# Kernel optimization log

Hardware: AMD Instinct MI355X
Metric: run time of the kernel (lower is better)

The kernel has to match this reference:

```python
import jax, jax.numpy as jnp
import numpy as np

N_NODES = 50000
N_EDGES = 800000
D = 64  # node_in = edge_out = node_out

def _mlp(h, w1, b1, w2, b2):
    h = jax.nn.relu(h @ w1 + b1)
    return h @ w2 + b2

def setup_inputs() -> dict:
    key = jax.random.key(0)
    ks = jax.random.split(key, 12)
    def lin(k, fan_in, fan_out):
        bound = 1.0 / np.sqrt(fan_in)
        kw, kb = jax.random.split(k)
        w = jax.random.uniform(kw, (fan_in, fan_out), jnp.float32, -bound, bound)
        b = jax.random.uniform(kb, (fan_out,), jnp.float32, -bound, bound)
        return w, b
    x = jax.random.normal(ks[0], (N_NODES, D), jnp.float32)
    edge_index = jax.random.randint(ks[1], (2, N_EDGES), 0, N_NODES, jnp.int64 if jax.config.jax_enable_x64 else jnp.int32)
    edge_attr = jax.random.normal(ks[2], (N_EDGES, D), jnp.float32)
    u = jax.random.normal(ks[3], (1, D), jnp.float32)
    batch = jnp.zeros((N_NODES,), dtype=edge_index.dtype)
    w1a, b1a = lin(ks[4], 2 * D, D)
    w1b, b1b = lin(ks[5], D, D)
    w2a, b2a = lin(ks[6], 2 * D, D)
    w2b, b2b = lin(ks[7], D, D)
    return dict(x=x, edge_index=edge_index, edge_attr=edge_attr, u=u, batch=batch,
                w1a=w1a, b1a=b1a, w1b=w1b, b1b=b1b,
                w2a=w2a, b2a=b2a, w2b=w2b, b2b=b2b)

def reference(x, edge_index, edge_attr, u, batch,
              w1a, b1a, w1b, b1b, w2a, b2a, w2b, b2b):
    row, col = edge_index[0], edge_index[1]
    n = x.shape[0]
    # gather source nodes, concat with edge features: [E, node_in+edge_out]
    h = jnp.concatenate([x[row], edge_attr], axis=1)
    h = _mlp(h, w1a, b1a, w1b, b1b)
    # scatter_mean over destination nodes (zeros for nodes with no incoming edges)
    summed = jax.ops.segment_sum(h, col, num_segments=n)  # [N, D]
    counts = jax.ops.segment_sum(jnp.ones((h.shape[0],), h.dtype), col, num_segments=n)
    agg = summed / jnp.maximum(counts, 1.0)[:, None]
    out = jnp.concatenate([x, agg], axis=1)
    return _mlp(out, w2a, b2a, w2b, b2b)
```

## Files before the change

kernel.cpp:

```cpp
#include <hip/hip_runtime.h>

#define DF 64

typedef __attribute__((ext_vector_type(8))) short bf16x8;
typedef __attribute__((ext_vector_type(2))) short v2s;
typedef __attribute__((ext_vector_type(4))) float f32x4;

__device__ __forceinline__ short f2bf(float f) {
    union { float f; unsigned u; } v; v.f = f;
    unsigned u = v.u;
    u += 0x7FFFu + ((u >> 16) & 1u);
    return (short)(u >> 16);
}

__device__ __forceinline__ float bf2f(unsigned s) {
    union { unsigned u; float f; } v; v.u = s << 16;
    return v.f;
}

__device__ __forceinline__ bf16x8 cvt8(float4 a, float4 b) {
    bf16x8 r;
    r[0] = f2bf(a.x); r[1] = f2bf(a.y); r[2] = f2bf(a.z); r[3] = f2bf(a.w);
    r[4] = f2bf(b.x); r[5] = f2bf(b.y); r[6] = f2bf(b.z); r[7] = f2bf(b.w);
    return r;
}

__device__ __forceinline__ void wave_lds_sync() {
    asm volatile("s_waitcnt lgkmcnt(0)" ::: "memory");
    __builtin_amdgcn_sched_barrier(0);
}

__device__ __forceinline__ void pk_add(short* addr, int val) {
#if __has_builtin(__builtin_amdgcn_global_atomic_fadd_v2bf16)
    __builtin_amdgcn_global_atomic_fadd_v2bf16(
        (__attribute__((address_space(1))) v2s*)addr, *(v2s*)&val);
#else
    unsigned* a = (unsigned*)addr;
    unsigned old = *a, assumed;
    do {
        assumed = old;
        float lo = bf2f(assumed & 0xffffu) + bf2f((unsigned)val & 0xffffu);
        float hi = bf2f(assumed >> 16)     + bf2f((unsigned)val >> 16);
        unsigned nv = (unsigned)(unsigned short)f2bf(lo) |
                      ((unsigned)(unsigned short)f2bf(hi) << 16);
        old = atomicCAS(a, assumed, nv);
    } while (old != assumed);
#endif
}

__global__ __launch_bounds__(256) void prep_weights(
    const float* __restrict__ w1a, const float* __restrict__ w1b,
    const float* __restrict__ w2a, const float* __restrict__ w2b,
    short* __restrict__ w1aT, short* __restrict__ w1bT,
    short* __restrict__ w2aT, short* __restrict__ w2bT)
{
    int gid = blockIdx.x * 256 + threadIdx.x;
    if (gid < 8192) {
        int k = gid >> 6, n = gid & 63;
        w1aT[n * 128 + k] = f2bf(w1a[gid]);
    } else if (gid < 12288) {
        int g = gid - 8192; int k = g >> 6, n = g & 63;
        w1bT[n * 64 + k] = f2bf(w1b[g]);
    } else if (gid < 20480) {
        int g = gid - 12288; int k = g >> 6, n = g & 63;
        w2aT[n * 128 + k] = f2bf(w2a[g]);
    } else if (gid < 24576) {
        int g = gid - 20480; int k = g >> 6, n = g & 63;
        w2bT[n * 64 + k] = f2bf(w2b[g]);
    }
}

__global__ __launch_bounds__(256, 4) void edge_mlp_scatter(
    const float* __restrict__ x, const int* __restrict__ ei,
    const float* __restrict__ ea,
    const short* __restrict__ w1aT, const float* __restrict__ b1a,
    const short* __restrict__ w1bT, const float* __restrict__ b1b,
    short* __restrict__ summedh, float* __restrict__ counts, int E)
{
    __shared__ alignas(16) short lsH[4 * 2 * 16 * 72];

    const int t = threadIdx.x;
    const int lane = t & 63;
    const int w = t >> 6;
    const int q = lane >> 4;
    const int m = lane & 15;
    const long base = ((long)blockIdx.x * 4 + w) * 32;

    const long e0 = base + m;
    const long e1 = base + 16 + m;
    const long ec0 = e0 < E ? e0 : (long)(E - 1);
    const long ec1 = e1 < E ? e1 : (long)(E - 1);
    const int row0 = ei[ec0];
    const int row1 = ei[ec1];

    if (q == 0) {
        if (e0 < E) unsafeAtomicAdd(&counts[ei[E + e0]], 1.0f);
        if (e1 < E) unsafeAtomicAdd(&counts[ei[E + e1]], 1.0f);
    }

    const float4* xr0 = (const float4*)(x + (long)row0 * DF);
    const float4* er0 = (const float4*)(ea + ec0 * DF);
    const float4* xr1 = (const float4*)(x + (long)row1 * DF);
    const float4* er1 = (const float4*)(ea + ec1 * DF);

    float4 ax0 = xr0[q * 2],     ax1 = xr0[q * 2 + 1];
    float4 ax2 = xr0[8 + q * 2], ax3 = xr0[8 + q * 2 + 1];
    float4 ae0 = er0[q * 2],     ae1 = er0[q * 2 + 1];
    float4 ae2 = er0[8 + q * 2], ae3 = er0[8 + q * 2 + 1];
    float4 bx0 = xr1[q * 2],     bx1 = xr1[q * 2 + 1];
    float4 bx2 = xr1[8 + q * 2], bx3 = xr1[8 + q * 2 + 1];
    float4 be0 = er1[q * 2],     be1 = er1[q * 2 + 1];
    float4 be2 = er1[8 + q * 2], be3 = er1[8 + q * 2 + 1];

    bf16x8 afr0[4], afr1[4];
    afr0[0] = cvt8(ax0, ax1); afr0[1] = cvt8(ax2, ax3);
    afr0[2] = cvt8(ae0, ae1); afr0[3] = cvt8(ae2, ae3);
    afr1[0] = cvt8(bx0, bx1); afr1[1] = cvt8(bx2, bx3);
    afr1[2] = cvt8(be0, be1); afr1[3] = cvt8(be2, be3);

    f32x4 acc0[4], acc1[4];
#pragma unroll
    for (int nt = 0; nt < 4; ++nt) {
        float b = b1a[nt * 16 + m];
        f32x4 v = {b, b, b, b};
        acc0[nt] = v; acc1[nt] = v;
#pragma unroll
        for (int ks = 0; ks < 4; ++ks) {
            bf16x8 wf = *(const bf16x8*)&w1aT[(nt * 16 + m) * 128 + ks * 32 + q * 8];
            acc0[nt] = __builtin_amdgcn_mfma_f32_16x16x32_bf16(afr0[ks], wf, acc0[nt], 0, 0, 0);
            acc1[nt] = __builtin_amdgcn_mfma_f32_16x16x32_bf16(afr1[ks], wf, acc1[nt], 0, 0, 0);
        }
    }

    short* hw0 = lsH + w * (2 * 16 * 72);
    short* hw1 = hw0 + 16 * 72;
#pragma unroll
    for (int nt = 0; nt < 4; ++nt)
#pragma unroll
        for (int r = 0; r < 4; ++r) {
            float v0 = acc0[nt][r] > 0.f ? acc0[nt][r] : 0.f;
            float v1 = acc1[nt][r] > 0.f ? acc1[nt][r] : 0.f;
            hw0[(q * 4 + r) * 72 + nt * 16 + m] = f2bf(v0);
            hw1[(q * 4 + r) * 72 + nt * 16 + m] = f2bf(v1);
        }
    wave_lds_sync();

    bf16x8 a20[2], a21[2];
    a20[0] = *(const bf16x8*)&hw0[m * 72 + q * 8];
    a20[1] = *(const bf16x8*)&hw0[m * 72 + 32 + q * 8];
    a21[0] = *(const bf16x8*)&hw1[m * 72 + q * 8];
    a21[1] = *(const bf16x8*)&hw1[m * 72 + 32 + q * 8];

    f32x4 acd0[4], acd1[4];
#pragma unroll
    for (int nt = 0; nt < 4; ++nt) {
        float b = b1b[nt * 16 + m];
        f32x4 v = {b, b, b, b};
        acd0[nt] = v; acd1[nt] = v;
#pragma unroll
        for (int ks = 0; ks < 2; ++ks) {
            bf16x8 wf = *(const bf16x8*)&w1bT[(nt * 16 + m) * 64 + ks * 32 + q * 8];
            acd0[nt] = __builtin_amdgcn_mfma_f32_16x16x32_bf16(a20[ks], wf, acd0[nt], 0, 0, 0);
            acd1[nt] = __builtin_amdgcn_mfma_f32_16x16x32_bf16(a21[ks], wf, acd1[nt], 0, 0, 0);
        }
    }
    wave_lds_sync();

#pragma unroll
    for (int nt = 0; nt < 4; ++nt)
#pragma unroll
        for (int r = 0; r < 4; ++r) {
            hw0[(q * 4 + r) * 72 + nt * 16 + m] = f2bf(acd0[nt][r]);
            hw1[(q * 4 + r) * 72 + nt * 16 + m] = f2bf(acd1[nt][r]);
        }
    wave_lds_sync();

    const int p = lane & 31;
    const int* hwi0 = (const int*)hw0;
    const int* hwi1 = (const int*)hw1;
#pragma unroll
    for (int i = 0; i < 8; ++i) {
        int r2 = (lane >> 5) + 2 * i;
        long eg0 = base + r2;
        long eg1 = base + 16 + r2;
        if (eg0 < E) {
            int dst = ei[E + eg0];
            pk_add(&summedh[(long)dst * DF + 2 * p], hwi0[r2 * 36 + p]);
        }
        if (eg1 < E) {
            int dst = ei[E + eg1];
            pk_add(&summedh[(long)dst * DF + 2 * p], hwi1[r2 * 36 + p]);
        }
    }
}

__global__ __launch_bounds__(256, 4) void node_mlp(
    const float* __restrict__ x, const short* __restrict__ summedh,
    const float* __restrict__ counts,
    const short* __restrict__ w2aT, const float* __restrict__ b2a,
    const short* __restrict__ w2bT, const float* __restrict__ b2b,
    float* __restrict__ out, int NN)
{
    __shared__ alignas(16) short lsH[4 * 2 * 16 * 72];

    const int t = threadIdx.x;
    const int lane = t & 63;
    const int w = t >> 6;
    const int q = lane >> 4;
    const int m = lane & 15;
    const long base = ((long)blockIdx.x * 4 + w) * 32;

    const long n0 = base + m;
    const long n1 = base + 16 + m;
    const long nc0 = n0 < NN ? n0 : (long)(NN - 1);
    const long nc1 = n1 < NN ? n1 : (long)(NN - 1);

    const float4* xr0 = (const float4*)(x + nc0 * DF);
    const float4* xr1 = (const float4*)(x + nc1 * DF);

    float4 ax0 = xr0[q * 2],     ax1 = xr0[q * 2 + 1];
    float4 ax2 = xr0[8 + q * 2], ax3 = xr0[8 + q * 2 + 1];
    float4 bx0 = xr1[q * 2],     bx1 = xr1[q * 2 + 1];
    float4 bx2 = xr1[8 + q * 2], bx3 = xr1[8 + q * 2 + 1];
    bf16x8 s00 = *(const bf16x8*)&summedh[nc0 * DF + q * 8];
    bf16x8 s01 = *(const bf16x8*)&summedh[nc0 * DF + 32 + q * 8];
    bf16x8 s10 = *(const bf16x8*)&summedh[nc1 * DF + q * 8];
    bf16x8 s11 = *(const bf16x8*)&summedh[nc1 * DF + 32 + q * 8];
    float c0 = counts[nc0];
    float c1 = counts[nc1];
    c0 = c0 > 1.f ? c0 : 1.f;
    c1 = c1 > 1.f ? c1 : 1.f;
    const float inv0 = 1.f / c0;
    const float inv1 = 1.f / c1;

    bf16x8 afr0[4], afr1[4];
    afr0[0] = cvt8(ax0, ax1); afr0[1] = cvt8(ax2, ax3);
    afr1[0] = cvt8(bx0, bx1); afr1[1] = cvt8(bx2, bx3);
#pragma unroll
    for (int i = 0; i < 8; ++i) {
        afr0[2][i] = f2bf(bf2f((unsigned short)s00[i]) * inv0);
        afr0[3][i] = f2bf(bf2f((unsigned short)s01[i]) * inv0);
        afr1[2][i] = f2bf(bf2f((unsigned short)s10[i]) * inv1);
        afr1[3][i] = f2bf(bf2f((unsigned short)s11[i]) * inv1);
    }

    f32x4 acc0[4], acc1[4];
#pragma unroll
    for (int nt = 0; nt < 4; ++nt) {
        float b = b2a[nt * 16 + m];
        f32x4 v = {b, b, b, b};
        acc0[nt] = v; acc1[nt] = v;
#pragma unroll
        for (int ks = 0; ks < 4; ++ks) {
            bf16x8 wf = *(const bf16x8*)&w2aT[(nt * 16 + m) * 128 + ks * 32 + q * 8];
            acc0[nt] = __builtin_amdgcn_mfma_f32_16x16x32_bf16(afr0[ks], wf, acc0[nt], 0, 0, 0);
            acc1[nt] = __builtin_amdgcn_mfma_f32_16x16x32_bf16(afr1[ks], wf, acc1[nt], 0, 0, 0);
        }
    }

    short* hw0 = lsH + w * (2 * 16 * 72);
    short* hw1 = hw0 + 16 * 72;
#pragma unroll
    for (int nt = 0; nt < 4; ++nt)
#pragma unroll
        for (int r = 0; r < 4; ++r) {
            float v0 = acc0[nt][r] > 0.f ? acc0[nt][r] : 0.f;
            float v1 = acc1[nt][r] > 0.f ? acc1[nt][r] : 0.f;
            hw0[(q * 4 + r) * 72 + nt * 16 + m] = f2bf(v0);
            hw1[(q * 4 + r) * 72 + nt * 16 + m] = f2bf(v1);
        }
    wave_lds_sync();

    bf16x8 a20[2], a21[2];
    a20[0] = *(const bf16x8*)&hw0[m * 72 + q * 8];
    a20[1] = *(const bf16x8*)&hw0[m * 72 + 32 + q * 8];
    a21[0] = *(const bf16x8*)&hw1[m * 72 + q * 8];
    a21[1] = *(const bf16x8*)&hw1[m * 72 + 32 + q * 8];

    f32x4 acd0[4], acd1[4];
#pragma unroll
    for (int nt = 0; nt < 4; ++nt) {
        float b = b2b[nt * 16 + m];
        f32x4 v = {b, b, b, b};
        acd0[nt] = v; acd1[nt] = v;
#pragma unroll
        for (int ks = 0; ks < 2; ++ks) {
            bf16x8 wf = *(const bf16x8*)&w2bT[(nt * 16 + m) * 64 + ks * 32 + q * 8];
            acd0[nt] = __builtin_amdgcn_mfma_f32_16x16x32_bf16(a20[ks], wf, acd0[nt], 0, 0, 0);
            acd1[nt] = __builtin_amdgcn_mfma_f32_16x16x32_bf16(a21[ks], wf, acd1[nt], 0, 0, 0);
        }
    }

#pragma unroll
    for (int r = 0; r < 4; ++r) {
        long o0 = base + q * 4 + r;
        long o1 = base + 16 + q * 4 + r;
        if (o0 < NN) {
#pragma unroll
            for (int nt = 0; nt < 4; ++nt)
                out[o0 * DF + nt * 16 + m] = acd0[nt][r];
        }
        if (o1 < NN) {
#pragma unroll
            for (int nt = 0; nt < 4; ++nt)
                out[o1 * DF + nt * 16 + m] = acd1[nt][r];
        }
    }
}

extern "C" void kernel_launch(void* const* d_in, const int* in_sizes, int n_in,
                              void* d_out, int out_size, void* d_ws, size_t ws_size,
                              hipStream_t stream) {
    const float* x   = (const float*)d_in[0];
    const int*   ei  = (const int*)d_in[1];
    const float* ea  = (const float*)d_in[2];
    const float* w1a = (const float*)d_in[5];
    const float* b1a = (const float*)d_in[6];
    const float* w1b = (const float*)d_in[7];
    const float* b1b = (const float*)d_in[8];
    const float* w2a = (const float*)d_in[9];
    const float* b2a = (const float*)d_in[10];
    const float* w2b = (const float*)d_in[11];
    const float* b2b = (const float*)d_in[12];

    const int NN = in_sizes[0] / DF;
    const int E  = in_sizes[2] / DF;

    char* wsb = (char*)d_ws;
    float* counts  = (float*)wsb;
    short* w1aT    = (short*)(wsb + 262144);
    short* w1bT    = (short*)(wsb + 278528);
    short* w2aT    = (short*)(wsb + 286720);
    short* w2bT    = (short*)(wsb + 303104);
    short* summedh = (short*)(wsb + 311296);

    hipMemsetAsync(counts, 0, (size_t)NN * sizeof(float), stream);
    hipMemsetAsync(summedh, 0, (size_t)NN * DF * sizeof(short), stream);
    prep_weights<<<96, 256, 0, stream>>>(w1a, w1b, w2a, w2b, w1aT, w1bT, w2aT, w2bT);

    int ewaves = (E + 31) / 32;
    int eblocks = (ewaves + 3) / 4;
    edge_mlp_scatter<<<eblocks, 256, 0, stream>>>(x, ei, ea, w1aT, b1a, w1bT, b1b,
                                                  summedh, counts, E);
    int nwaves = (NN + 31) / 32;
    int nblocks = (nwaves + 3) / 4;
    node_mlp<<<nblocks, 256, 0, stream>>>(x, summedh, counts, w2aT, b2a, w2bT, b2b,
                                          (float*)d_out, NN);
}
```

Measured before the change: 439.6 us.

## Replace atomic scatter-add with counting-sort of edge outputs and segmented node reduction

Builds a CSR layout of edges by destination using a histogram, a single-block scan and per-edge atomic cursors. The edge MLP writes each bf16 result row to its sorted slot instead of atomically adding into per-node sums, and the node kernel reduces its contiguous segment before the node MLP. This removes contended bf16 atomic adds in exchange for extra histogram and scan kernels, a slow one-block scan, and an E×64 bf16 intermediate buffer. The change only applies when the workspace is large enough, otherwise the old path runs.

```diff
diff --git a/kernel.cpp b/kernel.cpp
--- a/kernel.cpp
+++ b/kernel.cpp
@@ -70,6 +70,346 @@
     }
 }
 
+
+__global__ __launch_bounds__(256) void histogram_k(
+    const int* __restrict__ ei, int* __restrict__ icounts, int E)
+{
+    int gid = blockIdx.x * 256 + threadIdx.x;
+    if (gid < E) atomicAdd(&icounts[ei[E + gid]], 1);
+}
+
+__global__ __launch_bounds__(1024) void scan_offsets(
+    const int* __restrict__ icounts, int* __restrict__ offsets,
+    int* __restrict__ cursor, int NN, int E)
+{
+    __shared__ int part[1024];
+    const int t = threadIdx.x;
+    const int chunk = (NN + 1023) / 1024;
+    const int s = t * chunk;
+    const int e = (s + chunk < NN) ? s + chunk : NN;
+    int sum = 0;
+    for (int i = s; i < e; ++i) sum += icounts[i];
+    part[t] = sum;
+    __syncthreads();
+    for (int off = 1; off < 1024; off <<= 1) {
+        int v = part[t];
+        int o = (t >= off) ? part[t - off] : 0;
+        __syncthreads();
+        part[t] = v + o;
+        __syncthreads();
+    }
+    int run = part[t] - sum;
+    for (int i = s; i < e; ++i) {
+        offsets[i] = run;
+        cursor[i]  = run;
+        run += icounts[i];
+    }
+    if (t == 0) offsets[NN] = E;
+}
+
+__global__ __launch_bounds__(256, 4) void edge_mlp_sorted(
+    const float* __restrict__ x, const int* __restrict__ ei,
+    const float* __restrict__ ea,
+    const short* __restrict__ w1aT, const float* __restrict__ b1a,
+    const short* __restrict__ w1bT, const float* __restrict__ b1b,
+    short* __restrict__ h_sorted, int* __restrict__ cursor, int E)
+{
+    __shared__ alignas(16) short lsH[4 * 2 * 16 * 72];
+
+    const int t = threadIdx.x;
+    const int lane = t & 63;
+    const int w = t >> 6;
+    const int q = lane >> 4;
+    const int m = lane & 15;
+    const long base = ((long)blockIdx.x * 4 + w) * 32;
+
+    const long e0 = base + m;
+    const long e1 = base + 16 + m;
+    const long ec0 = e0 < E ? e0 : (long)(E - 1);
+    const long ec1 = e1 < E ? e1 : (long)(E - 1);
+    const int row0 = ei[ec0];
+    const int row1 = ei[ec1];
+
+    int pos = 0;
+    if (lane < 32) {
+        long eg = base + lane;
+        if (eg < E) pos = atomicAdd(&cursor[ei[E + eg]], 1);
+    }
+
+    const float4* xr0 = (const float4*)(x + (long)row0 * DF);
+    const float4* er0 = (const float4*)(ea + ec0 * DF);
+    const float4* xr1 = (const float4*)(x + (long)row1 * DF);
+    const float4* er1 = (const float4*)(ea + ec1 * DF);
+
+    float4 ax0 = xr0[q * 2],     ax1 = xr0[q * 2 + 1];
+    float4 ax2 = xr0[8 + q * 2], ax3 = xr0[8 + q * 2 + 1];
+    float4 ae0 = er0[q * 2],     ae1 = er0[q * 2 + 1];
+    float4 ae2 = er0[8 + q * 2], ae3 = er0[8 + q * 2 + 1];
+    float4 bx0 = xr1[q * 2],     bx1 = xr1[q * 2 + 1];
+    float4 bx2 = xr1[8 + q * 2], bx3 = xr1[8 + q * 2 + 1];
+    float4 be0 = er1[q * 2],     be1 = er1[q * 2 + 1];
+    float4 be2 = er1[8 + q * 2], be3 = er1[8 + q * 2 + 1];
+
+    bf16x8 afr0[4], afr1[4];
+    afr0[0] = cvt8(ax0, ax1); afr0[1] = cvt8(ax2, ax3);
+    afr0[2] = cvt8(ae0, ae1); afr0[3] = cvt8(ae2, ae3);
+    afr1[0] = cvt8(bx0, bx1); afr1[1] = cvt8(bx2, bx3);
+    afr1[2] = cvt8(be0, be1); afr1[3] = cvt8(be2, be3);
+
+    f32x4 acc0[4], acc1[4];
+#pragma unroll
+    for (int nt = 0; nt < 4; ++nt) {
+        float b = b1a[nt * 16 + m];
+        f32x4 v = {b, b, b, b};
+        acc0[nt] = v; acc1[nt] = v;
+#pragma unroll
+        for (int ks = 0; ks < 4; ++ks) {
+            bf16x8 wf = *(const bf16x8*)&w1aT[(nt * 16 + m) * 128 + ks * 32 + q * 8];
+            acc0[nt] = __builtin_amdgcn_mfma_f32_16x16x32_bf16(afr0[ks], wf, acc0[nt], 0, 0, 0);
+            acc1[nt] = __builtin_amdgcn_mfma_f32_16x16x32_bf16(afr1[ks], wf, acc1[nt], 0, 0, 0);
+        }
+    }
+
+    short* hw0 = lsH + w * (2 * 16 * 72);
+    short* hw1 = hw0 + 16 * 72;
+#pragma unroll
+    for (int nt = 0; nt < 4; ++nt)
+#pragma unroll
+        for (int r = 0; r < 4; ++r) {
+            float v0 = acc0[nt][r] > 0.f ? acc0[nt][r] : 0.f;
+            float v1 = acc1[nt][r] > 0.f ? acc1[nt][r] : 0.f;
+            hw0[(q * 4 + r) * 72 + nt * 16 + m] = f2bf(v0);
+            hw1[(q * 4 + r) * 72 + nt * 16 + m] = f2bf(v1);
+        }
+    wave_lds_sync();
+
+    bf16x8 a20[2], a21[2];
+    a20[0] = *(const bf16x8*)&hw0[m * 72 + q * 8];
+    a20[1] = *(const bf16x8*)&hw0[m * 72 + 32 + q * 8];
+    a21[0] = *(const bf16x8*)&hw1[m * 72 + q * 8];
+    a21[1] = *(const bf16x8*)&hw1[m * 72 + 32 + q * 8];
+
+    f32x4 acd0[4], acd1[4];
+#pragma unroll
+    for (int nt = 0; nt < 4; ++nt) {
+        float b = b1b[nt * 16 + m];
+        f32x4 v = {b, b, b, b};
+        acd0[nt] = v; acd1[nt] = v;
+#pragma unroll
+        for (int ks = 0; ks < 2; ++ks) {
+            bf16x8 wf = *(const bf16x8*)&w1bT[(nt * 16 + m) * 64 + ks * 32 + q * 8];
+            acd0[nt] = __builtin_amdgcn_mfma_f32_16x16x32_bf16(a20[ks], wf, acd0[nt], 0, 0, 0);
+            acd1[nt] = __builtin_amdgcn_mfma_f32_16x16x32_bf16(a21[ks], wf, acd1[nt], 0, 0, 0);
+        }
+    }
+    wave_lds_sync();
+
+#pragma unroll
+    for (int nt = 0; nt < 4; ++nt)
+#pragma unroll
+        for (int r = 0; r < 4; ++r) {
+            hw0[(q * 4 + r) * 72 + nt * 16 + m] = f2bf(acd0[nt][r]);
+            hw1[(q * 4 + r) * 72 + nt * 16 + m] = f2bf(acd1[nt][r]);
+        }
+    wave_lds_sync();
+
+    const int* hwi0 = (const int*)hw0;
+    const int* hwi1 = (const int*)hw1;
+    int* hs = (int*)h_sorted;
+#pragma unroll
+    for (int i = 0; i < 2; ++i) {
+        int r = (lane >> 3) + 8 * i;
+        int posr0 = __shfl(pos, r);
+        int posr1 = __shfl(pos, 16 + r);
+        if (base + r < E) {
+            int4 v = *(const int4*)&hwi0[r * 36 + (lane & 7) * 4];
+            *(int4*)&hs[(long)posr0 * 32 + (lane & 7) * 4] = v;
+        }
+        if (base + 16 + r < E) {
+            int4 v = *(const int4*)&hwi1[r * 36 + (lane & 7) * 4];
+            *(int4*)&hs[(long)posr1 * 32 + (lane & 7) * 4] = v;
+        }
+    }
+}
+
+__global__ __launch_bounds__(256, 4) void node_mlp_sorted(
+    const float* __restrict__ x, const short* __restrict__ h_sorted,
+    const int* __restrict__ offsets,
+    const short* __restrict__ w2aT, const float* __restrict__ b2a,
+    const short* __restrict__ w2bT, const float* __restrict__ b2b,
+    float* __restrict__ out, int NN)
+{
+    __shared__ alignas(16) short lsH[4 * 2 * 16 * 72];
+
+    const int t = threadIdx.x;
+    const int lane = t & 63;
+    const int w = t >> 6;
+    const int q = lane >> 4;
+    const int m = lane & 15;
+    const long base = ((long)blockIdx.x * 4 + w) * 32;
+
+    const long n0 = base + m;
+    const long n1 = base + 16 + m;
+    const long nc0 = n0 < NN ? n0 : (long)(NN - 1);
+    const long nc1 = n1 < NN ? n1 : (long)(NN - 1);
+
+    const int s0a = offsets[nc0];
+    const int cnt0 = offsets[nc0 + 1] - s0a;
+    const int s1a = offsets[nc1];
+    const int cnt1 = offsets[nc1 + 1] - s1a;
+    const float inv0 = 1.f / (float)(cnt0 > 1 ? cnt0 : 1);
+    const float inv1 = 1.f / (float)(cnt1 > 1 ? cnt1 : 1);
+
+    const float4* xr0 = (const float4*)(x + nc0 * DF);
+    const float4* xr1 = (const float4*)(x + nc1 * DF);
+    float4 ax0 = xr0[q * 2],     ax1 = xr0[q * 2 + 1];
+    float4 ax2 = xr0[8 + q * 2], ax3 = xr0[8 + q * 2 + 1];
+    float4 bx0 = xr1[q * 2],     bx1 = xr1[q * 2 + 1];
+    float4 bx2 = xr1[8 + q * 2], bx3 = xr1[8 + q * 2 + 1];
+
+    float fa0[8], fa1[8], fb0[8], fb1[8];
+#pragma unroll
+    for (int i = 0; i < 8; ++i) { fa0[i] = 0.f; fa1[i] = 0.f; fb0[i] = 0.f; fb1[i] = 0.f; }
+
+    {
+        int j = 0;
+        for (; j + 4 <= cnt0; j += 4) {
+            const short* rp = &h_sorted[(long)(s0a + j) * DF];
+            bf16x8 r0a = *(const bf16x8*)&rp[q * 8];
+            bf16x8 r0b = *(const bf16x8*)&rp[32 + q * 8];
+            bf16x8 r1a = *(const bf16x8*)&rp[64 + q * 8];
+            bf16x8 r1b = *(const bf16x8*)&rp[96 + q * 8];
+            bf16x8 r2a = *(const bf16x8*)&rp[128 + q * 8];
+            bf16x8 r2b = *(const bf16x8*)&rp[160 + q * 8];
+            bf16x8 r3a = *(const bf16x8*)&rp[192 + q * 8];
+            bf16x8 r3b = *(const bf16x8*)&rp[224 + q * 8];
+#pragma unroll
+            for (int i = 0; i < 8; ++i) {
+                fa0[i] += (bf2f((unsigned short)r0a[i]) + bf2f((unsigned short)r1a[i]))
+                        + (bf2f((unsigned short)r2a[i]) + bf2f((unsigned short)r3a[i]));
+                fa1[i] += (bf2f((unsigned short)r0b[i]) + bf2f((unsigned short)r1b[i]))
+                        + (bf2f((unsigned short)r2b[i]) + bf2f((unsigned short)r3b[i]));
+            }
+        }
+        for (; j < cnt0; ++j) {
+            const short* rp = &h_sorted[(long)(s0a + j) * DF];
+            bf16x8 ra = *(const bf16x8*)&rp[q * 8];
+            bf16x8 rb = *(const bf16x8*)&rp[32 + q * 8];
+#pragma unroll
+            for (int i = 0; i < 8; ++i) {
+                fa0[i] += bf2f((unsigned short)ra[i]);
+                fa1[i] += bf2f((unsigned short)rb[i]);
+            }
+        }
+    }
+    {
+        int j = 0;
+        for (; j + 4 <= cnt1; j += 4) {
+            const short* rp = &h_sorted[(long)(s1a + j) * DF];
+            bf16x8 r0a = *(const bf16x8*)&rp[q * 8];
+            bf16x8 r0b = *(const bf16x8*)&rp[32 + q * 8];
+            bf16x8 r1a = *(const bf16x8*)&rp[64 + q * 8];
+            bf16x8 r1b = *(const bf16x8*)&rp[96 + q * 8];
+            bf16x8 r2a = *(const bf16x8*)&rp[128 + q * 8];
+            bf16x8 r2b = *(const bf16x8*)&rp[160 + q * 8];
+            bf16x8 r3a = *(const bf16x8*)&rp[192 + q * 8];
+            bf16x8 r3b = *(const bf16x8*)&rp[224 + q * 8];
+#pragma unroll
+            for (int i = 0; i < 8; ++i) {
+                fb0[i] += (bf2f((unsigned short)r0a[i]) + bf2f((unsigned short)r1a[i]))
+                        + (bf2f((unsigned short)r2a[i]) + bf2f((unsigned short)r3a[i]));
+                fb1[i] += (bf2f((unsigned short)r0b[i]) + bf2f((unsigned short)r1b[i]))
+                        + (bf2f((unsigned short)r2b[i]) + bf2f((unsigned short)r3b[i]));
+            }
+        }
+        for (; j < cnt1; ++j) {
+            const short* rp = &h_sorted[(long)(s1a + j) * DF];
+            bf16x8 ra = *(const bf16x8*)&rp[q * 8];
+            bf16x8 rb = *(const bf16x8*)&rp[32 + q * 8];
+#pragma unroll
+            for (int i = 0; i < 8; ++i) {
+                fb0[i] += bf2f((unsigned short)ra[i]);
+                fb1[i] += bf2f((unsigned short)rb[i]);
+            }
+        }
+    }
+
+    bf16x8 afr0[4], afr1[4];
+    afr0[0] = cvt8(ax0, ax1); afr0[1] = cvt8(ax2, ax3);
+    afr1[0] = cvt8(bx0, bx1); afr1[1] = cvt8(bx2, bx3);
+#pragma unroll
+    for (int i = 0; i < 8; ++i) {
+        afr0[2][i] = f2bf(fa0[i] * inv0);
+        afr0[3][i] = f2bf(fa1[i] * inv0);
+        afr1[2][i] = f2bf(fb0[i] * inv1);
+        afr1[3][i] = f2bf(fb1[i] * inv1);
+    }
+
+    f32x4 acc0[4], acc1[4];
+#pragma unroll
+    for (int nt = 0; nt < 4; ++nt) {
+        float b = b2a[nt * 16 + m];
+        f32x4 v = {b, b, b, b};
+        acc0[nt] = v; acc1[nt] = v;
+#pragma unroll
+        for (int ks = 0; ks < 4; ++ks) {
+            bf16x8 wf = *(const bf16x8*)&w2aT[(nt * 16 + m) * 128 + ks * 32 + q * 8];
+            acc0[nt] = __builtin_amdgcn_mfma_f32_16x16x32_bf16(afr0[ks], wf, acc0[nt], 0, 0, 0);
+            acc1[nt] = __builtin_amdgcn_mfma_f32_16x16x32_bf16(afr1[ks], wf, acc1[nt], 0, 0, 0);
+        }
+    }
+
+    short* hw0 = lsH + w * (2 * 16 * 72);
+    short* hw1 = hw0 + 16 * 72;
+#pragma unroll
+    for (int nt = 0; nt < 4; ++nt)
+#pragma unroll
+        for (int r = 0; r < 4; ++r) {
+            float v0 = acc0[nt][r] > 0.f ? acc0[nt][r] : 0.f;
+            float v1 = acc1[nt][r] > 0.f ? acc1[nt][r] : 0.f;
+            hw0[(q * 4 + r) * 72 + nt * 16 + m] = f2bf(v0);
+            hw1[(q * 4 + r) * 72 + nt * 16 + m] = f2bf(v1);
+        }
+    wave_lds_sync();
+
+    bf16x8 a20[2], a21[2];
+    a20[0] = *(const bf16x8*)&hw0[m * 72 + q * 8];
+    a20[1] = *(const bf16x8*)&hw0[m * 72 + 32 + q * 8];
+    a21[0] = *(const bf16x8*)&hw1[m * 72 + q * 8];
+    a21[1] = *(const bf16x8*)&hw1[m * 72 + 32 + q * 8];
+
+    f32x4 acd0[4], acd1[4];
+#pragma unroll
+    for (int nt = 0; nt < 4; ++nt) {
+        float b = b2b[nt * 16 + m];
+        f32x4 v = {b, b, b, b};
+        acd0[nt] = v; acd1[nt] = v;
+#pragma unroll
+        for (int ks = 0; ks < 2; ++ks) {
+            bf16x8 wf = *(const bf16x8*)&w2bT[(nt * 16 + m) * 64 + ks * 32 + q * 8];
+            acd0[nt] = __builtin_amdgcn_mfma_f32_16x16x32_bf16(a20[ks], wf, acd0[nt], 0, 0, 0);
+            acd1[nt] = __builtin_amdgcn_mfma_f32_16x16x32_bf16(a21[ks], wf, acd1[nt], 0, 0, 0);
+        }
+    }
+
+#pragma unroll
+    for (int r = 0; r < 4; ++r) {
+        long o0 = base + q * 4 + r;
+        long o1 = base + 16 + q * 4 + r;
+        if (o0 < NN) {
+#pragma unroll
+            for (int nt = 0; nt < 4; ++nt)
+                out[o0 * DF + nt * 16 + m] = acd0[nt][r];
+        }
+        if (o1 < NN) {
+#pragma unroll
+            for (int nt = 0; nt < 4; ++nt)
+                out[o1 * DF + nt * 16 + m] = acd1[nt][r];
+        }
+    }
+}
+
+
 __global__ __launch_bounds__(256, 4) void edge_mlp_scatter(
     const float* __restrict__ x, const int* __restrict__ ei,
     const float* __restrict__ ea,
@@ -308,6 +648,7 @@
     }
 }
 
+
 extern "C" void kernel_launch(void* const* d_in, const int* in_sizes, int n_in,
                               void* d_out, int out_size, void* d_ws, size_t ws_size,
                               hipStream_t stream) {
@@ -327,23 +668,46 @@
     const int E  = in_sizes[2] / DF;
 
     char* wsb = (char*)d_ws;
-    float* counts  = (float*)wsb;
-    short* w1aT    = (short*)(wsb + 262144);
-    short* w1bT    = (short*)(wsb + 278528);
-    short* w2aT    = (short*)(wsb + 286720);
-    short* w2bT    = (short*)(wsb + 303104);
-    short* summedh = (short*)(wsb + 311296);
-
-    hipMemsetAsync(counts, 0, (size_t)NN * sizeof(float), stream);
-    hipMemsetAsync(summedh, 0, (size_t)NN * DF * sizeof(short), stream);
-    prep_weights<<<96, 256, 0, stream>>>(w1a, w1b, w2a, w2b, w1aT, w1bT, w2aT, w2bT);
+    const size_t need_sorted = 1048576 + (size_t)E * DF * sizeof(short);
 
     int ewaves = (E + 31) / 32;
     int eblocks = (ewaves + 3) / 4;
-    edge_mlp_scatter<<<eblocks, 256, 0, stream>>>(x, ei, ea, w1aT, b1a, w1bT, b1b,
-                                                  summedh, counts, E);
     int nwaves = (NN + 31) / 32;
     int nblocks = (nwaves + 3) / 4;
-    node_mlp<<<nblocks, 256, 0, stream>>>(x, summedh, counts, w2aT, b2a, w2bT, b2b,
-                                          (float*)d_out, NN);
-}
+
+    if (ws_size >= need_sorted) {
+        int*   icounts = (int*)wsb;
+        int*   offsets = (int*)(wsb + 262144);
+        int*   cursor  = (int*)(wsb + 524288);
+        short* w1aT    = (short*)(wsb + 786432);
+        short* w1bT    = (short*)(wsb + 802816);
+        short* w2aT    = (short*)(wsb + 811008);
+        short* w2bT    = (short*)(wsb + 827392);
+        short* h_sorted= (short*)(wsb + 1048576);
+
+        hipMemsetAsync(icounts, 0, (size_t)NN * sizeof(int), stream);
+        prep_weights<<<96, 256, 0, stream>>>(w1a, w1b, w2a, w2b, w1aT, w1bT, w2aT, w2bT);
+        histogram_k<<<(E + 255) / 256, 256, 0, stream>>>(ei, icounts, E);
+        scan_offsets<<<1, 1024, 0, stream>>>(icounts, offsets, cursor, NN, E);
+        edge_mlp_sorted<<<eblocks, 256, 0, stream>>>(x, ei, ea, w1aT, b1a, w1bT, b1b,
+                                                     h_sorted, cursor, E);
+        node_mlp_sorted<<<nblocks, 256, 0, stream>>>(x, h_sorted, offsets,
+                                                     w2aT, b2a, w2bT, b2b,
+                                                     (float*)d_out, NN);
+    } else {
+        float* counts  = (float*)wsb;
+        short* w1aT    = (short*)(wsb + 262144);
+        short* w1bT    = (short*)(wsb + 278528);
+        short* w2aT    = (short*)(wsb + 286720);
+        short* w2bT    = (short*)(wsb + 303104);
+        short* summedh = (short*)(wsb + 311296);
+
+        hipMemsetAsync(counts, 0, (size_t)NN * sizeof(float), stream);
+        hipMemsetAsync(summedh, 0, (size_t)NN * DF * sizeof(short), stream);
+        prep_weights<<<96, 256, 0, stream>>>(w1a, w1b, w2a, w2b, w1aT, w1bT, w2aT, w2bT);
+        edge_mlp_scatter<<<eblocks, 256, 0, stream>>>(x, ei, ea, w1aT, b1a, w1bT, b1b,
+                                                      summedh, counts, E);
+        node_mlp<<<nblocks, 256, 0, stream>>>(x, summedh, counts, w2aT, b2a, w2bT, b2b,
+                                              (float*)d_out, NN);
+    }
+}
```

Result: slower. 565.8 us (+28.7%).

## Use persistent edge kernel with prefetch pipeline, LDS-resident weights, bf16 x copy

Applied to the files above, without the earlier changes.

Replaces the one-shot edge kernel with a persistent grid-strided kernel. Each wave handles 16-edge tiles and prefetches the next tile's indices and features while computing the current one. Weights are staged once per block into swizzled LDS instead of being re-read from global memory per tile. A new pre-pass converts x to bf16 so the edge gathers and node kernel read half the bytes. The costs are an extra kernel launch plus a pass over x, and lower occupancy (launch bounds 3) from the 32KB LDS weight buffer.

```diff
diff --git a/kernel.cpp b/kernel.cpp
--- a/kernel.cpp
+++ b/kernel.cpp
@@ -70,12 +70,182 @@
     }
 }
 
-__global__ __launch_bounds__(256, 4) void edge_mlp_scatter(
-    const float* __restrict__ x, const int* __restrict__ ei,
+__global__ __launch_bounds__(256) void conv_x(
+    const float* __restrict__ x, short* __restrict__ xbf, int n8)
+{
+    int gid = blockIdx.x * 256 + threadIdx.x;
+    if (gid < n8) {
+        const float4* p = (const float4*)x + (long)gid * 2;
+        float4 a = p[0], b = p[1];
+        ((bf16x8*)xbf)[gid] = cvt8(a, b);
+    }
+}
+
+__global__ __launch_bounds__(256, 3) void edge_mlp_pipe(
+    const short* __restrict__ xbf, const int* __restrict__ ei,
     const float* __restrict__ ea,
-    const short* __restrict__ w1aT, const float* __restrict__ b1a,
-    const short* __restrict__ w1bT, const float* __restrict__ b1b,
-    short* __restrict__ summedh, float* __restrict__ counts, int E)
+    const short* __restrict__ w1aTg, const float* __restrict__ b1a,
+    const short* __restrict__ w1bTg, const float* __restrict__ b1b,
+    short* __restrict__ summedh, float* __restrict__ counts,
+    int E, int NT, int NWV)
+{
+    __shared__ alignas(16) char  lsW[32768];
+    __shared__ alignas(16) short lsH[4 * 16 * 72];
+
+    const int t = threadIdx.x;
+    const int lane = t & 63;
+    const int w = t >> 6;
+    const int q = lane >> 4;
+    const int m = lane & 15;
+    short* hw = lsH + w * (16 * 72);
+    const int* hwi = (const int*)hw;
+
+    {
+        const int4* g1 = (const int4*)w1aTg;
+        for (int c = t; c < 1024; c += 256) {
+            int b = c << 4;
+            *(int4*)(lsW + (b ^ (((b >> 8) & 15) << 4))) = g1[c];
+        }
+        const int4* g2 = (const int4*)w1bTg;
+        for (int c = t; c < 512; c += 256) {
+            int b = c << 4;
+            int pb = ((b >> 7) << 8) | (b & 127);
+            *(int4*)(lsW + 16384 + (pb ^ (((pb >> 8) & 15) << 4))) = g2[c];
+        }
+    }
+    float ba[4], bb[4];
+#pragma unroll
+    for (int nt = 0; nt < 4; ++nt) { ba[nt] = b1a[nt * 16 + m]; bb[nt] = b1b[nt * 16 + m]; }
+    __syncthreads();
+
+    long pA = (long)blockIdx.x * 4 + w;
+    if (pA >= NT) return;
+
+    long eA = pA * 16 + m;
+    long ecA = eA < E ? eA : (long)(E - 1);
+    int rA = ei[ecA];
+    int dA = ei[E + ecA];
+
+    long pB = pA + NWV;
+    long ecB = 0;
+    int rB = 0, dB = 0;
+    if (pB < NT) {
+        long eB = pB * 16 + m;
+        ecB = eB < E ? eB : (long)(E - 1);
+        rB = ei[ecB];
+        dB = ei[E + ecB];
+    }
+
+    bf16x8 xa0A, xa1A; float4 e0A, e1A, e2A, e3A;
+    {
+        const short* xr = xbf + (long)rA * DF;
+        xa0A = *(const bf16x8*)&xr[q * 8];
+        xa1A = *(const bf16x8*)&xr[32 + q * 8];
+        const float4* er = (const float4*)(ea + ecA * DF);
+        e0A = er[q * 2]; e1A = er[q * 2 + 1];
+        e2A = er[8 + q * 2]; e3A = er[8 + q * 2 + 1];
+    }
+
+    for (;;) {
+        bf16x8 xa0B, xa1B; float4 e0B, e1B, e2B, e3B;
+        if (pB < NT) {
+            const short* xr = xbf + (long)rB * DF;
+            xa0B = *(const bf16x8*)&xr[q * 8];
+            xa1B = *(const bf16x8*)&xr[32 + q * 8];
+            const float4* er = (const float4*)(ea + ecB * DF);
+            e0B = er[q * 2]; e1B = er[q * 2 + 1];
+            e2B = er[8 + q * 2]; e3B = er[8 + q * 2 + 1];
+        }
+        long pC = pB + NWV;
+        long ecC = 0;
+        int rC = 0, dC = 0;
+        if (pC < NT) {
+            long eC = pC * 16 + m;
+            ecC = eC < E ? eC : (long)(E - 1);
+            rC = ei[ecC];
+            dC = ei[E + ecC];
+        }
+
+        const long base = pA * 16;
+        if (q == 0 && eA < E) unsafeAtomicAdd(&counts[dA], 1.0f);
+
+        bf16x8 afr[4];
+        afr[0] = xa0A; afr[1] = xa1A;
+        afr[2] = cvt8(e0A, e1A); afr[3] = cvt8(e2A, e3A);
+
+        f32x4 acc[4];
+#pragma unroll
+        for (int nt = 0; nt < 4; ++nt) {
+            f32x4 v = {ba[nt], ba[nt], ba[nt], ba[nt]};
+            acc[nt] = v;
+#pragma unroll
+            for (int ks = 0; ks < 4; ++ks) {
+                const bf16x8 wf = *(const bf16x8*)(lsW +
+                    (((nt * 16 + m) << 8) + ((((ks) << 6) | (q << 4)) ^ (m << 4))));
+                acc[nt] = __builtin_amdgcn_mfma_f32_16x16x32_bf16(afr[ks], wf, acc[nt], 0, 0, 0);
+            }
+        }
+
+#pragma unroll
+        for (int nt = 0; nt < 4; ++nt)
+#pragma unroll
+            for (int r = 0; r < 4; ++r) {
+                float v = acc[nt][r] > 0.f ? acc[nt][r] : 0.f;
+                hw[(q * 4 + r) * 72 + nt * 16 + m] = f2bf(v);
+            }
+        wave_lds_sync();
+
+        bf16x8 a2[2];
+        a2[0] = *(const bf16x8*)&hw[m * 72 + q * 8];
+        a2[1] = *(const bf16x8*)&hw[m * 72 + 32 + q * 8];
+
+        f32x4 acd[4];
+#pragma unroll
+        for (int nt = 0; nt < 4; ++nt) {
+            f32x4 v = {bb[nt], bb[nt], bb[nt], bb[nt]};
+            acd[nt] = v;
+#pragma unroll
+            for (int ks = 0; ks < 2; ++ks) {
+                const bf16x8 wf = *(const bf16x8*)(lsW + 16384 +
+                    (((nt * 16 + m) << 8) + ((((ks) << 6) | (q << 4)) ^ (m << 4))));
+                acd[nt] = __builtin_amdgcn_mfma_f32_16x16x32_bf16(a2[ks], wf, acd[nt], 0, 0, 0);
+            }
+        }
+        wave_lds_sync();
+
+#pragma unroll
+        for (int nt = 0; nt < 4; ++nt)
+#pragma unroll
+            for (int r = 0; r < 4; ++r)
+                hw[(q * 4 + r) * 72 + nt * 16 + m] = f2bf(acd[nt][r]);
+        wave_lds_sync();
+
+        const int pp = lane & 31;
+#pragma unroll
+        for (int i = 0; i < 8; ++i) {
+            int r2 = (lane >> 5) + 2 * i;
+            long eg = base + r2;
+            if (eg < E) {
+                int dst = __shfl(dA, r2);
+                pk_add(&summedh[(long)dst * DF + 2 * pp], hwi[r2 * 36 + pp]);
+            }
+        }
+        wave_lds_sync();
+
+        if (pB >= NT) break;
+        pA = pB; eA = pA * 16 + m; rA = rB; dA = dB;
+        xa0A = xa0B; xa1A = xa1B;
+        e0A = e0B; e1A = e1B; e2A = e2B; e3A = e3B;
+        pB = pC; ecB = ecC; rB = rC; dB = dC;
+    }
+}
+
+__global__ __launch_bounds__(256, 4) void node_mlp(
+    const short* __restrict__ xbf, const short* __restrict__ summedh,
+    const float* __restrict__ counts,
+    const short* __restrict__ w2aT, const float* __restrict__ b2a,
+    const short* __restrict__ w2bT, const float* __restrict__ b2b,
+    float* __restrict__ out, int NN)
 {
     __shared__ alignas(16) short lsH[4 * 2 * 16 * 72];
 
@@ -86,142 +256,16 @@
     const int m = lane & 15;
     const long base = ((long)blockIdx.x * 4 + w) * 32;
 
-    const long e0 = base + m;
-    const long e1 = base + 16 + m;
-    const long ec0 = e0 < E ? e0 : (long)(E - 1);
-    const long ec1 = e1 < E ? e1 : (long)(E - 1);
-    const int row0 = ei[ec0];
-    const int row1 = ei[ec1];
-
-    if (q == 0) {
-        if (e0 < E) unsafeAtomicAdd(&counts[ei[E + e0]], 1.0f);
-        if (e1 < E) unsafeAtomicAdd(&counts[ei[E + e1]], 1.0f);
-    }
-
-    const float4* xr0 = (const float4*)(x + (long)row0 * DF);
-    const float4* er0 = (const float4*)(ea + ec0 * DF);
-    const float4* xr1 = (const float4*)(x + (long)row1 * DF);
-    const float4* er1 = (const float4*)(ea + ec1 * DF);
-
-    float4 ax0 = xr0[q * 2],     ax1 = xr0[q * 2 + 1];
-    float4 ax2 = xr0[8 + q * 2], ax3 = xr0[8 + q * 2 + 1];
-    float4 ae0 = er0[q * 2],     ae1 = er0[q * 2 + 1];
-    float4 ae2 = er0[8 + q * 2], ae3 = er0[8 + q * 2 + 1];
-    float4 bx0 = xr1[q * 2],     bx1 = xr1[q * 2 + 1];
-    float4 bx2 = xr1[8 + q * 2], bx3 = xr1[8 + q * 2 + 1];
-    float4 be0 = er1[q * 2],     be1 = er1[q * 2 + 1];
-    float4 be2 = er1[8 + q * 2], be3 = er1[8 + q * 2 + 1];
-
-    bf16x8 afr0[4], afr1[4];
-    afr0[0] = cvt8(ax0, ax1); afr0[1] = cvt8(ax2, ax3);
-    afr0[2] = cvt8(ae0, ae1); afr0[3] = cvt8(ae2, ae3);
-    afr1[0] = cvt8(bx0, bx1); afr1[1] = cvt8(bx2, bx3);
-    afr1[2] = cvt8(be0, be1); afr1[3] = cvt8(be2, be3);
-
-    f32x4 acc0[4], acc1[4];
-#pragma unroll
-    for (int nt = 0; nt < 4; ++nt) {
-        float b = b1a[nt * 16 + m];
-        f32x4 v = {b, b, b, b};
-        acc0[nt] = v; acc1[nt] = v;
-#pragma unroll
-        for (int ks = 0; ks < 4; ++ks) {
-            bf16x8 wf = *(const bf16x8*)&w1aT[(nt * 16 + m) * 128 + ks * 32 + q * 8];
-            acc0[nt] = __builtin_amdgcn_mfma_f32_16x16x32_bf16(afr0[ks], wf, acc0[nt], 0, 0, 0);
-            acc1[nt] = __builtin_amdgcn_mfma_f32_16x16x32_bf16(afr1[ks], wf, acc1[nt], 0, 0, 0);
-        }
-    }
-
-    short* hw0 = lsH + w * (2 * 16 * 72);
-    short* hw1 = hw0 + 16 * 72;
-#pragma unroll
-    for (int nt = 0; nt < 4; ++nt)
-#pragma unroll
-        for (int r = 0; r < 4; ++r) {
-            float v0 = acc0[nt][r] > 0.f ? acc0[nt][r] : 0.f;
-            float v1 = acc1[nt][r] > 0.f ? acc1[nt][r] : 0.f;
-            hw0[(q * 4 + r) * 72 + nt * 16 + m] = f2bf(v0);
-            hw1[(q * 4 + r) * 72 + nt * 16 + m] = f2bf(v1);
-        }
-    wave_lds_sync();
-
-    bf16x8 a20[2], a21[2];
-    a20[0] = *(const bf16x8*)&hw0[m * 72 + q * 8];
-    a20[1] = *(const bf16x8*)&hw0[m * 72 + 32 + q * 8];
-    a21[0] = *(const bf16x8*)&hw1[m * 72 + q * 8];
-    a21[1] = *(const bf16x8*)&hw1[m * 72 + 32 + q * 8];
-
-    f32x4 acd0[4], acd1[4];
-#pragma unroll
-    for (int nt = 0; nt < 4; ++nt) {
-        float b = b1b[nt * 16 + m];
-        f32x4 v = {b, b, b, b};
-        acd0[nt] = v; acd1[nt] = v;
-#pragma unroll
-        for (int ks = 0; ks < 2; ++ks) {
-            bf16x8 wf = *(const bf16x8*)&w1bT[(nt * 16 + m) * 64 + ks * 32 + q * 8];
-            acd0[nt] = __builtin_amdgcn_mfma_f32_16x16x32_bf16(a20[ks], wf, acd0[nt], 0, 0, 0);
-            acd1[nt] = __builtin_amdgcn_mfma_f32_16x16x32_bf16(a21[ks], wf, acd1[nt], 0, 0, 0);
-        }
-    }
-    wave_lds_sync();
-
-#pragma unroll
-    for (int nt = 0; nt < 4; ++nt)
-#pragma unroll
-        for (int r = 0; r < 4; ++r) {
-            hw0[(q * 4 + r) * 72 + nt * 16 + m] = f2bf(acd0[nt][r]);
-            hw1[(q * 4 + r) * 72 + nt * 16 + m] = f2bf(acd1[nt][r]);
-        }
-    wave_lds_sync();
-
-    const int p = lane & 31;
-    const int* hwi0 = (const int*)hw0;
-    const int* hwi1 = (const int*)hw1;
-#pragma unroll
-    for (int i = 0; i < 8; ++i) {
-        int r2 = (lane >> 5) + 2 * i;
-        long eg0 = base + r2;
-        long eg1 = base + 16 + r2;
-        if (eg0 < E) {
-            int dst = ei[E + eg0];
-            pk_add(&summedh[(long)dst * DF + 2 * p], hwi0[r2 * 36 + p]);
-        }
-        if (eg1 < E) {
-            int dst = ei[E + eg1];
-            pk_add(&summedh[(long)dst * DF + 2 * p], hwi1[r2 * 36 + p]);
-        }
-    }
-}
-
-__global__ __launch_bounds__(256, 4) void node_mlp(
-    const float* __restrict__ x, const short* __restrict__ summedh,
-    const float* __restrict__ counts,
-    const short* __restrict__ w2aT, const float* __restrict__ b2a,
-    const short* __restrict__ w2bT, const float* __restrict__ b2b,
-    float* __restrict__ out, int NN)
-{
-    __shared__ alignas(16) short lsH[4 * 2 * 16 * 72];
-
-    const int t = threadIdx.x;
-    const int lane = t & 63;
-    const int w = t >> 6;
-    const int q = lane >> 4;
-    const int m = lane & 15;
-    const long base = ((long)blockIdx.x * 4 + w) * 32;
-
     const long n0 = base + m;
     const long n1 = base + 16 + m;
     const long nc0 = n0 < NN ? n0 : (long)(NN - 1);
     const long nc1 = n1 < NN ? n1 : (long)(NN - 1);
 
-    const float4* xr0 = (const float4*)(x + nc0 * DF);
-    const float4* xr1 = (const float4*)(x + nc1 * DF);
-
-    float4 ax0 = xr0[q * 2],     ax1 = xr0[q * 2 + 1];
-    float4 ax2 = xr0[8 + q * 2], ax3 = xr0[8 + q * 2 + 1];
-    float4 bx0 = xr1[q * 2],     bx1 = xr1[q * 2 + 1];
-    float4 bx2 = xr1[8 + q * 2], bx3 = xr1[8 + q * 2 + 1];
+    bf16x8 afr0[4], afr1[4];
+    afr0[0] = *(const bf16x8*)&xbf[nc0 * DF + q * 8];
+    afr0[1] = *(const bf16x8*)&xbf[nc0 * DF + 32 + q * 8];
+    afr1[0] = *(const bf16x8*)&xbf[nc1 * DF + q * 8];
+    afr1[1] = *(const bf16x8*)&xbf[nc1 * DF + 32 + q * 8];
     bf16x8 s00 = *(const bf16x8*)&summedh[nc0 * DF + q * 8];
     bf16x8 s01 = *(const bf16x8*)&summedh[nc0 * DF + 32 + q * 8];
     bf16x8 s10 = *(const bf16x8*)&summedh[nc1 * DF + q * 8];
@@ -233,9 +277,6 @@
     const float inv0 = 1.f / c0;
     const float inv1 = 1.f / c1;
 
-    bf16x8 afr0[4], afr1[4];
-    afr0[0] = cvt8(ax0, ax1); afr0[1] = cvt8(ax2, ax3);
-    afr1[0] = cvt8(bx0, bx1); afr1[1] = cvt8(bx2, bx3);
 #pragma unroll
     for (int i = 0; i < 8; ++i) {
         afr0[2][i] = f2bf(bf2f((unsigned short)s00[i]) * inv0);
@@ -307,6 +348,7 @@
         }
     }
 }
+
 
 extern "C" void kernel_launch(void* const* d_in, const int* in_sizes, int n_in,
                               void* d_out, int out_size, void* d_ws, size_t ws_size,
@@ -333,17 +375,21 @@
     short* w2aT    = (short*)(wsb + 286720);
     short* w2bT    = (short*)(wsb + 303104);
     short* summedh = (short*)(wsb + 311296);
+    short* xbf     = (short*)(wsb + 6815744);
 
     hipMemsetAsync(counts, 0, (size_t)NN * sizeof(float), stream);
     hipMemsetAsync(summedh, 0, (size_t)NN * DF * sizeof(short), stream);
     prep_weights<<<96, 256, 0, stream>>>(w1a, w1b, w2a, w2b, w1aT, w1bT, w2aT, w2bT);
-
-    int ewaves = (E + 31) / 32;
-    int eblocks = (ewaves + 3) / 4;
-    edge_mlp_scatter<<<eblocks, 256, 0, stream>>>(x, ei, ea, w1aT, b1a, w1bT, b1b,
-                                                  summedh, counts, E);
+    int n8 = NN * DF / 8;
+    conv_x<<<(n8 + 255) / 256, 256, 0, stream>>>(x, xbf, n8);
+
+    const int EBLOCKS = 768;
+    const int NT = (E + 15) / 16;
+    edge_mlp_pipe<<<EBLOCKS, 256, 0, stream>>>(xbf, ei, ea, w1aT, b1a, w1bT, b1b,
+                                               summedh, counts, E, NT, EBLOCKS * 4);
+
     int nwaves = (NN + 31) / 32;
     int nblocks = (nwaves + 3) / 4;
-    node_mlp<<<nblocks, 256, 0, stream>>>(x, summedh, counts, w2aT, b2a, w2bT, b2b,
+    node_mlp<<<nblocks, 256, 0, stream>>>(xbf, summedh, counts, w2aT, b2a, w2bT, b2b,
                                           (float*)d_out, NN);
 }
```

New measurement: 400.4 us. 1.1x faster.
